# Optimization experiments

Hardware: AMD Instinct MI355X
Metric: run time of the kernel (lower is better)

Reference implementation:

```python
import jax, jax.numpy as jnp
import numpy as np

NUM_HEADS = 12

def setup_inputs() -> dict:
    key = jax.random.key(0)
    ks = jax.random.split(key, 6)
    B, N, C = 16, 1024, 768
    H, d = NUM_HEADS, C // NUM_HEADS
    return {
        "x": jax.random.normal(ks[0], (B, N, C), dtype=jnp.float32),
        "W_qkv": jax.random.normal(ks[1], (C, 3 * C), dtype=jnp.float32) * 0.02,
        "b_qkv": jax.random.normal(ks[2], (3 * C,), dtype=jnp.float32) * 0.02,
        "zeta": jnp.ones((1, 1, H, 1, d), dtype=jnp.float32),
        "W_proj": jax.random.normal(ks[3], (C, C), dtype=jnp.float32) * 0.02,
        "b_proj": jax.random.normal(ks[4], (C,), dtype=jnp.float32) * 0.02,
        "mask": jnp.zeros((B, N), dtype=bool),
    }

def reference(x, W_qkv, b_qkv, zeta, W_proj, b_proj, mask):
    B, N, C = x.shape
    H = NUM_HEADS
    d = C // H
    scale = d ** -0.5
    # qkv: (B,N,3C) -> (B,N,3,H,d) -> (3,B,H,N,d), gated by zeta (1,1,H,1,d)
    qkv = (x @ W_qkv + b_qkv).reshape(B, N, 3, H, d).transpose(2, 0, 3, 1, 4)
    qkv = qkv * zeta
    q, k, v = qkv[0], qkv[1], qkv[2]
    attn = jnp.einsum("bhnd,bhmd->bhnm", q, k) * scale
    # mask (B,N) over keys -> (B,1,1,N)
    attn = jnp.where(mask[:, None, None, :], -jnp.inf, attn)
    attn = jax.nn.softmax(attn, axis=-1)
    out = jnp.einsum("bhnm,bhmd->bhnd", attn, v)          # (B,H,N,d)
    out = out.transpose(0, 2, 1, 3).reshape(B, N, C)
    return out @ W_proj + b_proj
```

## Files before the change

### kernel.cpp

```cpp
#include <hip/hip_runtime.h>
#include <hip/hip_bf16.h>

typedef unsigned short ushort_t;
typedef __bf16 bf16_t;
typedef bf16_t bf16x8 __attribute__((ext_vector_type(8)));
typedef float floatx4 __attribute__((ext_vector_type(4)));
typedef ushort_t ushortx8 __attribute__((ext_vector_type(8)));

struct alignas(8) us4 { ushort_t x, y, z, w; };

__device__ __forceinline__ ushort_t f2bf(float f) {
  union { float f; unsigned int u; } v; v.f = f;
  unsigned int u = v.u;
  return (ushort_t)((u + 0x7fffu + ((u >> 16) & 1u)) >> 16);
}

__device__ __forceinline__ unsigned int pk_bf16(float a, float b) {
  __hip_bfloat162 h = __float22bfloat162_rn(float2{a, b});
  union { __hip_bfloat162 h; unsigned int u; } v; v.h = h;
  return v.u;
}

__device__ __forceinline__ void async16(const void* g, void* l) {
  __builtin_amdgcn_global_load_lds(
      (const __attribute__((address_space(1))) unsigned int*)g,
      (__attribute__((address_space(3))) unsigned int*)l, 16, 0, 0);
}

#define LOG2E 1.44269504088896340736f


__global__ __launch_bounds__(256) void k_prep(const float* __restrict__ x,
                                              ushort_t* __restrict__ xb,
                                              const float* __restrict__ Wq,
                                              ushort_t* __restrict__ WqT,
                                              const float* __restrict__ Wp,
                                              ushort_t* __restrict__ WpT) {
  __shared__ float tile[32][33];
  const int bid = blockIdx.x, t = threadIdx.x;
  if (bid < 6144) {
    size_t i = ((size_t)bid * 256 + t) * 8;
    float4 a = *(const float4*)(x + i);
    float4 b = *(const float4*)(x + i + 4);
    ushortx8 o;
    o[0] = f2bf(a.x); o[1] = f2bf(a.y); o[2] = f2bf(a.z); o[3] = f2bf(a.w);
    o[4] = f2bf(b.x); o[5] = f2bf(b.y); o[6] = f2bf(b.z); o[7] = f2bf(b.w);
    *(ushortx8*)(xb + i) = o;
    return;
  }
  const float* in; ushort_t* out; int C, c0, r0;
  if (bid < 7872) {
    int b2 = bid - 6144;
    in = Wq; out = WqT; C = 2304;
    c0 = (b2 % 72) * 32; r0 = (b2 / 72) * 32;
  } else {
    int b3 = bid - 7872;
    in = Wp; out = WpT; C = 768;
    c0 = (b3 % 24) * 32; r0 = (b3 / 24) * 32;
  }
  const int tx = t & 31, ty = t >> 5;
#pragma unroll
  for (int i = 0; i < 32; i += 8)
    tile[ty + i][tx] = in[(size_t)(r0 + ty + i) * C + c0 + tx];
  __syncthreads();
#pragma unroll
  for (int i = 0; i < 32; i += 8)
    out[(size_t)(c0 + ty + i) * 768 + r0 + tx] = f2bf(tile[tx][ty + i]);
}


__device__ __forceinline__ void gemm_bt_dbuf(const ushort_t* __restrict__ A,
                                             const ushort_t* __restrict__ Bt,
                                             int m0, int n0,
                                             ushort_t* sA, ushort_t* sB,
                                             floatx4 acc[4][4]) {
  const int t = threadIdx.x;
  const int lane = t & 63, w = t >> 6;
  const int wr = w >> 1, wc = w & 1;
  const int lr = lane & 15, qd = lane >> 4;
  const int swz = ((t & 3) ^ ((t >> 3) & 3)) * 8;
  const ushort_t* gA = A + (size_t)(m0 + (t >> 2)) * 768 + swz;
  const ushort_t* gB = Bt + (size_t)(n0 + (t >> 2)) * 768 + swz;
  char* lA = (char*)sA + t * 16;
  char* lB = (char*)sB + t * 16;
  const int rsz = (qd ^ ((lr >> 1) & 3)) * 16;
  async16(gA, lA);
  async16(gA + 64 * 768, lA + 4096);
  async16(gB, lB);
  async16(gB + 64 * 768, lB + 4096);
  asm volatile("s_waitcnt vmcnt(0)" ::: "memory");
  __syncthreads();
#pragma unroll 2
  for (int k = 0; k < 24; ++k) {
    const int p = k & 1, pn = p ^ 1;
    if (k < 23) {
      const int k0 = (k + 1) * 32;
      async16(gA + k0, lA + pn * 8192);
      async16(gA + k0 + 64 * 768, lA + pn * 8192 + 4096);
      async16(gB + k0, lB + pn * 8192);
      async16(gB + k0 + 64 * 768, lB + pn * 8192 + 4096);
    }
    const char* cA = (const char*)sA + p * 8192;
    const char* cB = (const char*)sB + p * 8192;
    bf16x8 af[4], bfr[4];
#pragma unroll
    for (int i = 0; i < 4; ++i)
      af[i] = *(const bf16x8*)(cA + (wr * 64 + i * 16 + lr) * 64 + rsz);
#pragma unroll
    for (int j = 0; j < 4; ++j)
      bfr[j] = *(const bf16x8*)(cB + (wc * 64 + j * 16 + lr) * 64 + rsz);
#pragma unroll
    for (int i = 0; i < 4; ++i)
#pragma unroll
      for (int j = 0; j < 4; ++j)
        acc[i][j] = __builtin_amdgcn_mfma_f32_16x16x32_bf16(af[i], bfr[j], acc[i][j], 0, 0, 0);
    asm volatile("s_waitcnt vmcnt(0)" ::: "memory");
    __syncthreads();
  }
}


__global__ __launch_bounds__(256, 4) void k_qkv(const ushort_t* __restrict__ xb,
                                                const ushort_t* __restrict__ WqT,
                                                const float* __restrict__ bqkv,
                                                const float* __restrict__ zeta,
                                                ushort_t* __restrict__ qb,
                                                ushort_t* __restrict__ kb,
                                                ushort_t* __restrict__ vtb) {
  __shared__ alignas(16) ushort_t sA[2 * 128 * 32];
  __shared__ alignas(16) ushort_t sB[2 * 128 * 32];
  floatx4 acc[4][4] = {};
  const int m0 = blockIdx.y * 128, n0 = blockIdx.x * 128;
  gemm_bt_dbuf(xb, WqT, m0, n0, sA, sB, acc);
  const int t = threadIdx.x, lane = t & 63, w = t >> 6;
  const int wr = w >> 1, wc = w & 1, lr = lane & 15, qd = lane >> 4;
  const int tq = n0 / 768;
#pragma unroll
  for (int j = 0; j < 4; ++j) {
    int n = n0 + wc * 64 + j * 16 + lr;
    int nc = n - tq * 768;
    int h = nc >> 6, dim = n & 63;
    float bias = bqkv[n];
    float zv = zeta[nc];
    float mult = (tq == 0) ? zv * 0.125f * LOG2E : zv;
    if (tq < 2) {
      ushort_t* dst = (tq == 0) ? qb : kb;
#pragma unroll
      for (int i = 0; i < 4; ++i) {
        int mbase = m0 + wr * 64 + i * 16 + qd * 4;
#pragma unroll
        for (int r = 0; r < 4; ++r) {
          int m = mbase + r;
          int b = m >> 10, seq = m & 1023;
          dst[(((size_t)b * 12 + h) * 1024 + seq) * 64 + dim] = f2bf((acc[i][j][r] + bias) * mult);
        }
      }
    } else {
#pragma unroll
      for (int i = 0; i < 4; ++i) {
        int mbase = m0 + wr * 64 + i * 16 + qd * 4;
        int b = mbase >> 10, seq = mbase & 1023;
        us4 pk;
        pk.x = f2bf((acc[i][j][0] + bias) * mult);
        pk.y = f2bf((acc[i][j][1] + bias) * mult);
        pk.z = f2bf((acc[i][j][2] + bias) * mult);
        pk.w = f2bf((acc[i][j][3] + bias) * mult);
        *(us4*)&vtb[(((size_t)b * 12 + h) * 64 + dim) * 1024 + seq] = pk;
      }
    }
  }
}


__global__ __launch_bounds__(256, 3) void k_attn(const ushort_t* __restrict__ qg,
                                                 const ushort_t* __restrict__ kg,
                                                 const ushort_t* __restrict__ vg,
                                                 const unsigned char* __restrict__ mask,
                                                 ushort_t* __restrict__ ob) {
  __shared__ alignas(16) char smem[49664];
  char* sV = smem + 32768;
  float* maskadd = (float*)(smem + 49152);
  const int t = threadIdx.x, lane = t & 63, w = t >> 6;
  const int lr = lane & 15, qd = lane >> 4;
  const int lin = blockIdx.x;
  const int bh = (lin & 7) + 8 * (lin >> 6);
  const int qt = (lin >> 3) & 7;
  const int b = bh / 12, h = bh % 12;
  const int qrow0 = qt * 128 + w * 32;
  const ushort_t* qp = qg + (size_t)bh * 65536;
  const ushort_t* kp = kg + (size_t)bh * 65536;
  const ushort_t* vp = vg + (size_t)bh * 65536;
  const unsigned char* mp = mask + b * 1024;

  bf16x8 qf[2][2];
#pragma unroll
  for (int ns = 0; ns < 2; ++ns)
#pragma unroll
    for (int kk = 0; kk < 2; ++kk)
      qf[ns][kk] = *(const bf16x8*)(qp + (size_t)(qrow0 + ns * 16 + lr) * 64 + kk * 32 + qd * 8);

  floatx4 o[4][2] = {};
  float lst[2] = {0.f, 0.f};
  char* sPw = smem + 16384 + w * 4096;

  for (int kt = 0; kt < 8; ++kt) {
    __syncthreads();
    const ushort_t* kpt = kp + kt * 8192;
#pragma unroll
    for (int it = 0; it < 4; ++it) {
      int p = it * 256 + t;
      int r = p >> 3, cs = (p & 7) ^ (r & 7);
      async16(kpt + r * 64 + cs * 8, smem + p * 16);
    }
    const ushort_t* vpt = vp + kt * 128;
#pragma unroll
    for (int it = 0; it < 4; ++it) {
      int p = it * 256 + t;
      int r = p >> 4, cs = (p & 15) ^ (r & 15);
      async16(vpt + (size_t)r * 1024 + cs * 8, sV + p * 16);
    }
    if (t < 128) maskadd[t] = mp[kt * 128 + t] ? -1e30f : 0.0f;
    asm volatile("s_waitcnt vmcnt(0)" ::: "memory");
    __syncthreads();

#pragma unroll
    for (int hh = 0; hh < 2; ++hh) {
      floatx4 s[4][2] = {};
#pragma unroll
      for (int kk = 0; kk < 2; ++kk) {
#pragma unroll
        for (int ms = 0; ms < 4; ++ms) {
          bf16x8 ak = *(const bf16x8*)(smem + ((hh * 4 + ms) * 16 + lr) * 128 +
                                       ((kk * 4 + qd) ^ (lr & 7)) * 16);
#pragma unroll
          for (int ns = 0; ns < 2; ++ns)
            s[ms][ns] = __builtin_amdgcn_mfma_f32_16x16x32_bf16(ak, qf[ns][kk], s[ms][ns], 0, 0, 0);
        }
      }
#pragma unroll
      for (int ms = 0; ms < 4; ++ms) {
        float4 mk = *(const float4*)&maskadd[(hh * 4 + ms) * 16 + qd * 4];
#pragma unroll
        for (int ns = 0; ns < 2; ++ns) {
          float p0 = __builtin_amdgcn_exp2f(s[ms][ns][0] + mk.x);
          float p1 = __builtin_amdgcn_exp2f(s[ms][ns][1] + mk.y);
          float p2 = __builtin_amdgcn_exp2f(s[ms][ns][2] + mk.z);
          float p3 = __builtin_amdgcn_exp2f(s[ms][ns][3] + mk.w);
          lst[ns] += (p0 + p1) + (p2 + p3);
          uint2 pk;
          pk.x = pk_bf16(p0, p1);
          pk.y = pk_bf16(p2, p3);
          *(uint2*)(sPw + (ns * 16 + lr) * 128 +
                    ((ms * 2 + (qd >> 1)) ^ (lr & 7)) * 16 + (qd & 1) * 8) = pk;
        }
      }
      asm volatile("s_waitcnt lgkmcnt(0)" ::: "memory");
#pragma unroll
      for (int kk = 0; kk < 2; ++kk) {
        bf16x8 pb[2];
#pragma unroll
        for (int ns = 0; ns < 2; ++ns)
          pb[ns] = *(const bf16x8*)(sPw + (ns * 16 + lr) * 128 +
                                    ((kk * 4 + qd) ^ (lr & 7)) * 16);
#pragma unroll
        for (int ds = 0; ds < 4; ++ds) {
          bf16x8 av = *(const bf16x8*)(sV + (ds * 16 + lr) * 256 +
                                       ((hh * 8 + kk * 4 + qd) ^ lr) * 16);
#pragma unroll
          for (int ns = 0; ns < 2; ++ns)
            o[ds][ns] = __builtin_amdgcn_mfma_f32_16x16x32_bf16(av, pb[ns], o[ds][ns], 0, 0, 0);
        }
      }
    }
  }
#pragma unroll
  for (int ns = 0; ns < 2; ++ns) {
    lst[ns] += __shfl_xor(lst[ns], 16);
    lst[ns] += __shfl_xor(lst[ns], 32);
  }
#pragma unroll
  for (int ns = 0; ns < 2; ++ns) {
    float rl = 1.0f / lst[ns];
    size_t row = (size_t)(b * 1024 + qrow0 + ns * 16 + lr) * 768 + h * 64;
#pragma unroll
    for (int ds = 0; ds < 4; ++ds) {
      uint2 ov;
      ov.x = pk_bf16(o[ds][ns][0] * rl, o[ds][ns][1] * rl);
      ov.y = pk_bf16(o[ds][ns][2] * rl, o[ds][ns][3] * rl);
      *(uint2*)&ob[row + ds * 16 + qd * 4] = ov;
    }
  }
}


__global__ __launch_bounds__(256, 4) void k_proj(const ushort_t* __restrict__ ob,
                                                 const ushort_t* __restrict__ WpT,
                                                 const float* __restrict__ bproj,
                                                 float* __restrict__ out) {
  __shared__ alignas(16) ushort_t sA[2 * 128 * 32];
  __shared__ alignas(16) ushort_t sB[2 * 128 * 32];
  floatx4 acc[4][4] = {};
  const int m0 = blockIdx.y * 128, n0 = blockIdx.x * 128;
  gemm_bt_dbuf(ob, WpT, m0, n0, sA, sB, acc);
  const int t = threadIdx.x, lane = t & 63, w = t >> 6;
  const int wr = w >> 1, wc = w & 1, lr = lane & 15, qd = lane >> 4;
#pragma unroll
  for (int j = 0; j < 4; ++j) {
    int n = n0 + wc * 64 + j * 16 + lr;
    float bias = bproj[n];
#pragma unroll
    for (int i = 0; i < 4; ++i) {
      int mbase = m0 + wr * 64 + i * 16 + qd * 4;
#pragma unroll
      for (int r = 0; r < 4; ++r)
        out[(size_t)(mbase + r) * 768 + n] = acc[i][j][r] + bias;
    }
  }
}


extern "C" void kernel_launch(void* const* d_in, const int* in_sizes, int n_in,
                              void* d_out, int out_size, void* d_ws, size_t ws_size,
                              hipStream_t stream) {
  const float* x = (const float*)d_in[0];
  const float* bqkv = (const float*)d_in[2];
  const float* zeta = (const float*)d_in[3];
  const float* bproj = (const float*)d_in[5];
  const unsigned char* mask = (const unsigned char*)d_in[6];
  float* out = (float*)d_out;
  char* ws = (char*)d_ws;
  ushort_t* xb  = (ushort_t*)(ws);
  ushort_t* WqT = (ushort_t*)(ws + 25165824);
  ushort_t* WpT = (ushort_t*)(ws + 28704768);
  ushort_t* qb  = (ushort_t*)(ws + 29884416);
  ushort_t* kb  = (ushort_t*)(ws + 55050240);
  ushort_t* vtb = (ushort_t*)(ws + 80216064);
  ushort_t* ob  = xb;

  k_prep<<<dim3(8448), dim3(256), 0, stream>>>(x, xb, (const float*)d_in[1], WqT,
                                               (const float*)d_in[4], WpT);
  k_qkv<<<dim3(18, 128), dim3(256), 0, stream>>>(xb, WqT, bqkv, zeta, qb, kb, vtb);
  k_attn<<<dim3(1536), dim3(256), 0, stream>>>(qb, kb, vtb, mask, ob);
  k_proj<<<dim3(6, 128), dim3(256), 0, stream>>>(ob, WpT, bproj, out);
}
```

Before: 307.4 us.

## Triple-buffer GEMM k-loop and remap blocks to XCD-grouped row tiles

Replaces the double-buffered GEMM mainloop with a three-stage async LDS pipeline that keeps two tiles in flight, using partial vmcnt waits and raw s_barrier instead of a full drain each step. Also linearizes the grid and remaps block ids so each XCD processes a contiguous band of row tiles, aiming for better L2 reuse of the A operand. The extra LDS buffer lowers the occupancy target from 4 to 3 blocks per CU.

Measured after the change: 290.5 us. 1.06x faster.

```diff
diff --git a/kernel.cpp b/kernel.cpp
--- a/kernel.cpp
+++ b/kernel.cpp
@@ -69,11 +69,11 @@
 }
 
 
-__device__ __forceinline__ void gemm_bt_dbuf(const ushort_t* __restrict__ A,
-                                             const ushort_t* __restrict__ Bt,
-                                             int m0, int n0,
-                                             ushort_t* sA, ushort_t* sB,
-                                             floatx4 acc[4][4]) {
+__device__ __forceinline__ void gemm_pipe3(const ushort_t* __restrict__ A,
+                                           const ushort_t* __restrict__ Bt,
+                                           int m0, int n0,
+                                           ushort_t* sA, ushort_t* sB,
+                                           floatx4 acc[4][4]) {
   const int t = threadIdx.x;
   const int lane = t & 63, w = t >> 6;
   const int wr = w >> 1, wc = w & 1;
@@ -84,24 +84,23 @@
   char* lA = (char*)sA + t * 16;
   char* lB = (char*)sB + t * 16;
   const int rsz = (qd ^ ((lr >> 1) & 3)) * 16;
-  async16(gA, lA);
-  async16(gA + 64 * 768, lA + 4096);
-  async16(gB, lB);
-  async16(gB + 64 * 768, lB + 4096);
-  asm volatile("s_waitcnt vmcnt(0)" ::: "memory");
-  __syncthreads();
-#pragma unroll 2
+#define ISSUE(kk, buf)                                    \
+  do {                                                    \
+    const int k0_ = (kk) * 32, b_ = (buf) * 8192;         \
+    async16(gA + k0_, lA + b_);                           \
+    async16(gA + k0_ + 64 * 768, lA + b_ + 4096);         \
+    async16(gB + k0_, lB + b_);                           \
+    async16(gB + k0_ + 64 * 768, lB + b_ + 4096);         \
+  } while (0)
+  ISSUE(0, 0);
+  ISSUE(1, 1);
+  asm volatile("s_waitcnt vmcnt(4)" ::: "memory");
+  asm volatile("s_barrier" ::: "memory");
+#pragma unroll
   for (int k = 0; k < 24; ++k) {
-    const int p = k & 1, pn = p ^ 1;
-    if (k < 23) {
-      const int k0 = (k + 1) * 32;
-      async16(gA + k0, lA + pn * 8192);
-      async16(gA + k0 + 64 * 768, lA + pn * 8192 + 4096);
-      async16(gB + k0, lB + pn * 8192);
-      async16(gB + k0 + 64 * 768, lB + pn * 8192 + 4096);
-    }
-    const char* cA = (const char*)sA + p * 8192;
-    const char* cB = (const char*)sB + p * 8192;
+    if (k + 2 < 24) ISSUE(k + 2, (k + 2) % 3);
+    const char* cA = (const char*)sA + (k % 3) * 8192;
+    const char* cB = (const char*)sB + (k % 3) * 8192;
     bf16x8 af[4], bfr[4];
 #pragma unroll
     for (int i = 0; i < 4; ++i)
@@ -114,24 +113,31 @@
 #pragma unroll
       for (int j = 0; j < 4; ++j)
         acc[i][j] = __builtin_amdgcn_mfma_f32_16x16x32_bf16(af[i], bfr[j], acc[i][j], 0, 0, 0);
-    asm volatile("s_waitcnt vmcnt(0)" ::: "memory");
-    __syncthreads();
-  }
-}
-
-
-__global__ __launch_bounds__(256, 4) void k_qkv(const ushort_t* __restrict__ xb,
+    if (k < 22)
+      asm volatile("s_waitcnt vmcnt(4)" ::: "memory");
+    else if (k == 22)
+      asm volatile("s_waitcnt vmcnt(0)" ::: "memory");
+    if (k < 23) asm volatile("s_barrier" ::: "memory");
+  }
+#undef ISSUE
+}
+
+
+__global__ __launch_bounds__(256, 3) void k_qkv(const ushort_t* __restrict__ xb,
                                                 const ushort_t* __restrict__ WqT,
                                                 const float* __restrict__ bqkv,
                                                 const float* __restrict__ zeta,
                                                 ushort_t* __restrict__ qb,
                                                 ushort_t* __restrict__ kb,
                                                 ushort_t* __restrict__ vtb) {
-  __shared__ alignas(16) ushort_t sA[2 * 128 * 32];
-  __shared__ alignas(16) ushort_t sB[2 * 128 * 32];
+  __shared__ alignas(16) ushort_t sA[3 * 4096];
+  __shared__ alignas(16) ushort_t sB[3 * 4096];
   floatx4 acc[4][4] = {};
-  const int m0 = blockIdx.y * 128, n0 = blockIdx.x * 128;
-  gemm_bt_dbuf(xb, WqT, m0, n0, sA, sB, acc);
+  const int lin = blockIdx.x;
+  const int xcd = lin & 7, idx = lin >> 3;
+  const int m0 = (xcd * 16 + (idx & 15)) * 128;
+  const int n0 = (idx >> 4) * 128;
+  gemm_pipe3(xb, WqT, m0, n0, sA, sB, acc);
   const int t = threadIdx.x, lane = t & 63, w = t >> 6;
   const int wr = w >> 1, wc = w & 1, lr = lane & 15, qd = lane >> 4;
   const int tq = n0 / 768;
@@ -293,15 +299,18 @@
 }
 
 
-__global__ __launch_bounds__(256, 4) void k_proj(const ushort_t* __restrict__ ob,
+__global__ __launch_bounds__(256, 3) void k_proj(const ushort_t* __restrict__ ob,
                                                  const ushort_t* __restrict__ WpT,
                                                  const float* __restrict__ bproj,
                                                  float* __restrict__ out) {
-  __shared__ alignas(16) ushort_t sA[2 * 128 * 32];
-  __shared__ alignas(16) ushort_t sB[2 * 128 * 32];
+  __shared__ alignas(16) ushort_t sA[3 * 4096];
+  __shared__ alignas(16) ushort_t sB[3 * 4096];
   floatx4 acc[4][4] = {};
-  const int m0 = blockIdx.y * 128, n0 = blockIdx.x * 128;
-  gemm_bt_dbuf(ob, WpT, m0, n0, sA, sB, acc);
+  const int lin = blockIdx.x;
+  const int xcd = lin & 7, idx = lin >> 3;
+  const int m0 = (xcd * 16 + (idx & 15)) * 128;
+  const int n0 = (idx >> 4) * 128;
+  gemm_pipe3(ob, WpT, m0, n0, sA, sB, acc);
   const int t = threadIdx.x, lane = t & 63, w = t >> 6;
   const int wr = w >> 1, wc = w & 1, lr = lane & 15, qd = lane >> 4;
 #pragma unroll
@@ -339,7 +348,7 @@
 
   k_prep<<<dim3(8448), dim3(256), 0, stream>>>(x, xb, (const float*)d_in[1], WqT,
                                                (const float*)d_in[4], WpT);
-  k_qkv<<<dim3(18, 128), dim3(256), 0, stream>>>(xb, WqT, bqkv, zeta, qb, kb, vtb);
+  k_qkv<<<dim3(2304), dim3(256), 0, stream>>>(xb, WqT, bqkv, zeta, qb, kb, vtb);
   k_attn<<<dim3(1536), dim3(256), 0, stream>>>(qb, kb, vtb, mask, ob);
-  k_proj<<<dim3(6, 128), dim3(256), 0, stream>>>(ob, WpT, bproj, out);
-}
+  k_proj<<<dim3(768), dim3(256), 0, stream>>>(ob, WpT, bproj, out);
+}
```
